# Performance work log

Hardware: AMD Instinct MI355X
Metric: run time of the kernel (lower is better)

The kernel has to match this reference:

```python
import jax, jax.numpy as jnp
import numpy as np
from jax import lax

B, FCH, H, W = 2, 48, 512, 512
WNUM, PATCH = 1, 8
DEG = 180.0 / np.pi
# well-conditioned, slightly asymmetric fallback Mueller matrix for masked (non-physical) pixels
_SAFE = np.array([[1.0, 0.02, 0.01, 0.005],
                  [0.0, 0.95, 0.05, 0.0],
                  [0.0, -0.05, 0.90, 0.04],
                  [0.0, 0.0, -0.04, 0.85]], dtype=np.float32)


def setup_inputs():
    key = jax.random.key(0)
    x = 0.5 * jax.random.normal(key, (B, FCH, H, W), dtype=jnp.float32)
    eye = jnp.eye(4, dtype=jnp.float32).reshape(16)
    # bias intensity frames and both calibration matrices toward 2*I so per-pixel
    # 4x4 systems are well conditioned and M is near-physical
    boost = jnp.concatenate([2.0 * eye, 2.0 * eye, 2.0 * eye])[None, :, None, None]
    return {"x": x + boost}


def _charpoly_mask(M):
    # Cloude realizability test: characteristic-polynomial coefficients of the
    # Hermitian coherency matrix must all be >= 0 (all eigenvalues >= 0).
    s = jnp.stack([jnp.eye(2, dtype=jnp.complex64),
                   jnp.array([[1, 0], [0, -1]], jnp.complex64),
                   jnp.array([[0, 1], [1, 0]], jnp.complex64),
                   jnp.array([[0, -1j], [1j, 0]], jnp.complex64)])
    Bk = jnp.einsum('iab,jcd->ijacbd', s, s).reshape(16, 4, 4)  # kron(sigma_i, sigma_j)
    Hc = 0.25 * jnp.einsum('...k,kab->...ab', M.reshape(M.shape[:-2] + (16,)).astype(jnp.complex64), Bk)
    tr1 = jnp.trace(Hc, axis1=-2, axis2=-1).real
    H2 = Hc @ Hc
    tr2 = jnp.trace(H2, axis1=-2, axis2=-1).real
    tr3 = jnp.trace(H2 @ Hc, axis1=-2, axis2=-1).real
    c2 = 0.5 * (tr1 ** 2 - tr2)
    c3 = (tr1 ** 3 - 3.0 * tr1 * tr2 + 2.0 * tr3) / 6.0
    c4 = jnp.linalg.det(Hc).real
    return (tr1 >= 0) & (c2 >= 0) & (c3 >= 0) & (c4 >= 0)


def _compute_mm(A, F, Wm, norm=True):
    M = jnp.linalg.solve(A, F)  # A^-1 F
    M = jnp.swapaxes(jnp.linalg.solve(jnp.swapaxes(Wm, -1, -2), jnp.swapaxes(M, -1, -2)), -1, -2)  # ... W^-1
    return M / M[..., 0:1, 0:1] if norm else M


def _lu_chipman(M, mask):
    # Lu-Chipman polar decomposition M = M_delta @ M_R @ M_D (per pixel)
    M = jnp.where(mask[..., None, None], M, jnp.asarray(_SAFE))
    I3 = jnp.eye(3, dtype=M.dtype)
    D = M[..., 0, 1:]  # diattenuation vector
    d2 = jnp.clip(jnp.sum(D * D, -1), 0.0, 1.0 - 1e-6)
    d = jnp.sqrt(d2 + 1e-12)
    sq = jnp.sqrt(1.0 - d2)
    Dh = D / jnp.maximum(d, 1e-6)[..., None]
    mD = sq[..., None, None] * I3 + (1.0 - sq)[..., None, None] * (Dh[..., :, None] * Dh[..., None, :])
    ones = jnp.ones(M.shape[:-2] + (1,), M.dtype)
    MD = jnp.concatenate([jnp.concatenate([ones, D], -1)[..., None, :],
                          jnp.concatenate([D[..., None], mD], -1)], -2)
    Mp = jnp.swapaxes(jnp.linalg.solve(MD, jnp.swapaxes(M, -1, -2)), -1, -2)  # M @ MD^-1 (MD symmetric)
    mp = Mp[..., 1:, 1:]
    mm = mp @ jnp.swapaxes(mp, -1, -2)
    lam = jnp.clip(jnp.linalg.eigvalsh(mm), 1e-12, None)  # ascending
    s1, s2, s3 = jnp.sqrt(lam[..., 2]), jnp.sqrt(lam[..., 1]), jnp.sqrt(lam[..., 0])
    sgn = jnp.where(jnp.linalg.det(mp) < 0, -1.0, 1.0).astype(M.dtype)
    A3 = mm + (s1 * s2 + s2 * s3 + s3 * s1)[..., None, None] * I3 + 1e-6 * I3
    B3 = (s1 + s2 + s3)[..., None, None] * mm + (s1 * s2 * s3)[..., None, None] * I3
    mdel = sgn[..., None, None] * jnp.linalg.solve(A3, B3)
    Pdel = (M[..., 1:, 0] - jnp.einsum('...ij,...j->...i', M[..., 1:, 1:], D)) / (1.0 - d2)[..., None]
    top = jnp.concatenate([ones, jnp.zeros(M.shape[:-2] + (3,), M.dtype)], -1)[..., None, :]
    Mdel = jnp.concatenate([top, jnp.concatenate([Pdel[..., None], mdel], -1)], -2)
    MR = jnp.linalg.solve(Mdel + 1e-6 * jnp.eye(4, dtype=M.dtype), Mp)
    return MD, MR, Mdel


def _polarimetry(MD, MR, Mdel):
    clipc = lambda t: jnp.clip(t, -1.0 + 1e-6, 1.0 - 1e-6)
    D = MD[..., 0, 1:]
    totD = jnp.sqrt(jnp.sum(D * D, -1) + 1e-12)
    linD = jnp.sqrt(D[..., 0] ** 2 + D[..., 1] ** 2 + 1e-12)
    cirD = jnp.abs(D[..., 2])
    totR = jnp.arccos(clipc(jnp.trace(MR, axis1=-2, axis2=-1) / 2.0 - 1.0)) * DEG
    mR = MR[..., 1:, 1:]
    linR = jnp.arccos(clipc(jnp.sqrt((mR[..., 0, 0] + mR[..., 1, 1]) ** 2
                                     + (mR[..., 1, 0] - mR[..., 0, 1]) ** 2 + 1e-12) - 1.0)) * DEG
    cirR = 0.5 * jnp.arctan2(mR[..., 1, 0] - mR[..., 0, 1], mR[..., 0, 0] + mR[..., 1, 1]) * DEG
    # azimuth of linear retardance from retardance-vector components (r1, r2)
    azi = jnp.mod(0.5 * jnp.arctan2(mR[..., 2, 0] - mR[..., 0, 2], mR[..., 1, 2] - mR[..., 2, 1]) * DEG, 180.0)
    dazi = jnp.mod(0.5 * jnp.arctan2(D[..., 1], D[..., 0]) * DEG, 180.0)
    totP = 1.0 - jnp.abs(jnp.trace(Mdel[..., 1:, 1:], axis1=-2, axis2=-1)) / 3.0
    # p[:,0]=diattenuation, p[:,6]=linear retardance, p[:,7]=azimuth, p[:,-1]=depolarization
    return jnp.stack([totD, linD, cirD, totR, cirR, dazi, linR, azi, totP], axis=1)


def _rolling_circstd(a_deg, patch):
    # circstd(a/180*pi, high=pi, low=0) over patch x patch sliding windows, back to degrees.
    # circstd reduces to window means of cos/sin of doubled angles -> avg pooling.
    th = a_deg * (2.0 * np.pi / 180.0)
    wsum = lambda t: lax.reduce_window(t, 0.0, lax.add, (1, 1, patch, patch), (1, 1, 1, 1), 'SAME')
    cnt = wsum(jnp.ones_like(a_deg))
    R = jnp.sqrt(wsum(jnp.cos(th)) ** 2 + wsum(jnp.sin(th)) ** 2 + 1e-12) / cnt
    R = jnp.clip(R, 1e-7, 1.0 - 1e-7)
    return 0.5 * jnp.sqrt(-2.0 * jnp.log(R)) * DEG


def _forward(x):
    b, f, h, w = x.shape
    xw = jnp.moveaxis(x.reshape(b, WNUM, f // WNUM, h, w), 2, -1)  # (b, wnum, h, w, 48)
    Fi = xw[..., :16].reshape(b, WNUM, h, w, 4, 4)
    Am = xw[..., 16:32].reshape(b, WNUM, h, w, 4, 4)
    Wm = xw[..., 32:48].reshape(b, WNUM, h, w, 4, 4)
    M = _compute_mm(Am, Fi, Wm, norm=True)
    inten = xw[..., 0]
    imin = inten.min(axis=(1, 2, 3), keepdims=True)
    imax = inten.max(axis=(1, 2, 3), keepdims=True)
    inorm = (inten - imin) / (imax - imin)
    mchan = jnp.moveaxis(M.reshape(b, WNUM, h, w, 16), -1, 2).reshape(b, WNUM * 16, h, w)
    v = lax.stop_gradient(_charpoly_mask(M))
    MD, MR, Mdel = _lu_chipman(M, v)
    p = _polarimetry(MD, MR, Mdel)  # (b, 9, wnum, h, w)
    std = _rolling_circstd(p[:, 7], PATCH)
    # concat order matches forward: intensity, mueller, linr, totp, datt, azimuth, std
    return jnp.concatenate([inorm, mchan, p[:, 6], p[:, 8], p[:, 0], p[:, 7], std], axis=1)


def reference(x):
    return _forward(x)
```

## Files before the change

kernel.cpp:

```cpp
#include <hip/hip_runtime.h>
#include <math.h>

#define B_ 2
#define H_ 512
#define W_ 512
#define HW_ (H_ * W_)
#define NCH_IN 48
#define NCH_OUT 22
#define DEG_ 57.29577951308232f

__device__ __forceinline__ float frcp(float x)  { return __builtin_amdgcn_rcpf(x); }
__device__ __forceinline__ float frcp_nr(float x) {
    float r = __builtin_amdgcn_rcpf(x);
    return r * __builtin_fmaf(-x, r, 2.0f);
}
__device__ __forceinline__ float fsqrtf_(float x){ return __builtin_amdgcn_sqrtf(x); }

__device__ __forceinline__ float fast_acos(float x) {
    float ax = fabsf(x);
    float t = fsqrtf_(fmaxf(1.0f - ax, 0.0f));
    float p = t * (1.5707288f + ax * (-0.2121144f + ax * (0.0742610f + ax * (-0.0187293f))));
    return (x >= 0.0f) ? p : (3.14159265358979f - p);
}

__device__ __forceinline__ float fast_atan2(float y, float x) {
    float ay = fabsf(y), ax = fabsf(x);
    float mx = fmaxf(ax, ay), mn = fminf(ax, ay);
    float a = mn * frcp(fmaxf(mx, 1e-37f));
    float s = a * a;
    float r = a * (0.99997726f + s * (-0.33262347f + s * (0.19354346f +
              s * (-0.11643287f + s * (0.05265332f + s * (-0.01172120f))))));
    if (ay > ax) r = 1.57079632679f - r;
    if (x < 0.0f) r = 3.14159265359f - r;
    return (y < 0.0f) ? -r : r;
}

__device__ __forceinline__ unsigned int fkey(float f) {
    unsigned int u = __float_as_uint(f);
    return (u & 0x80000000u) ? ~u : (u | 0x80000000u);
}
__device__ __forceinline__ float funkey(unsigned int k) {
    return (k & 0x80000000u) ? __uint_as_float(k ^ 0x80000000u) : __uint_as_float(~k);
}

__global__ __launch_bounds__(256) void minmax_kernel(const float* __restrict__ x,
                                                     unsigned int* __restrict__ mm) {
    int b = blockIdx.x >> 6;
    int blk = blockIdx.x & 63;
    const float* src = x + (size_t)b * NCH_IN * HW_;
    float lo = INFINITY, hi = -INFINITY;
    for (int i = blk * 256 + threadIdx.x; i < HW_; i += 64 * 256) {
        float v = src[i];
        lo = fminf(lo, v);
        hi = fmaxf(hi, v);
    }
    __shared__ float slo[256], shi[256];
    slo[threadIdx.x] = lo; shi[threadIdx.x] = hi;
    __syncthreads();
    for (int s = 128; s > 0; s >>= 1) {
        if (threadIdx.x < s) {
            slo[threadIdx.x] = fminf(slo[threadIdx.x], slo[threadIdx.x + s]);
            shi[threadIdx.x] = fmaxf(shi[threadIdx.x], shi[threadIdx.x + s]);
        }
        __syncthreads();
    }
    if (threadIdx.x == 0) {
        atomicMax(&mm[2 * b], ~fkey(slo[0]));
        atomicMax(&mm[2 * b + 1], fkey(shi[0]));
    }
}

__device__ __forceinline__ void solve4_dual(float m[2][4][8]) {
#pragma unroll
    for (int k = 0; k < 4; k++) {
#pragma unroll
        for (int r = k + 1; r < 4; r++) {
#pragma unroll
            for (int q = 0; q < 2; q++) {
                bool sw = fabsf(m[q][r][k]) > fabsf(m[q][k][k]);
#pragma unroll
                for (int c = k; c < 8; c++) {
                    float a = m[q][k][c], b = m[q][r][c];
                    m[q][k][c] = sw ? b : a;
                    m[q][r][c] = sw ? a : b;
                }
            }
        }
        float piv[2];
#pragma unroll
        for (int q = 0; q < 2; q++) piv[q] = frcp_nr(m[q][k][k]);
#pragma unroll
        for (int c = k + 1; c < 8; c++) {
#pragma unroll
            for (int q = 0; q < 2; q++) m[q][k][c] *= piv[q];
        }
#pragma unroll
        for (int r = 0; r < 4; r++) {
            if (r == k) continue;
#pragma unroll
            for (int q = 0; q < 2; q++) {
                float f = m[q][r][k];
#pragma unroll
                for (int c = k + 1; c < 8; c++)
                    m[q][r][c] = __builtin_fmaf(-f, m[q][k][c], m[q][r][c]);
            }
        }
    }
}

__device__ __forceinline__ void mul4(const float A[4][4], const float B[4][4], float C[4][4]) {
#pragma unroll
    for (int i = 0; i < 4; i++)
#pragma unroll
        for (int j = 0; j < 4; j++) {
            float s = 0.0f;
#pragma unroll
            for (int k = 0; k < 4; k++) s += A[i][k] * B[k][j];
            C[i][j] = s;
        }
}

__device__ __forceinline__ void inv3(const float A[3][3], float out[3][3]) {
    float c00 = A[1][1] * A[2][2] - A[1][2] * A[2][1];
    float c01 = A[1][2] * A[2][0] - A[1][0] * A[2][2];
    float c02 = A[1][0] * A[2][1] - A[1][1] * A[2][0];
    float det = A[0][0] * c00 + A[0][1] * c01 + A[0][2] * c02;
    float id = frcp_nr(det);
    out[0][0] = c00 * id;
    out[0][1] = (A[0][2] * A[2][1] - A[0][1] * A[2][2]) * id;
    out[0][2] = (A[0][1] * A[1][2] - A[0][2] * A[1][1]) * id;
    out[1][0] = c01 * id;
    out[1][1] = (A[0][0] * A[2][2] - A[0][2] * A[2][0]) * id;
    out[1][2] = (A[0][2] * A[1][0] - A[0][0] * A[1][2]) * id;
    out[2][0] = c02 * id;
    out[2][1] = (A[0][1] * A[2][0] - A[0][0] * A[2][1]) * id;
    out[2][2] = (A[0][0] * A[1][1] - A[0][1] * A[1][0]) * id;
}

__device__ __forceinline__ float det3(const float A[3][3]) {
    return A[0][0] * (A[1][1] * A[2][2] - A[1][2] * A[2][1])
         - A[0][1] * (A[1][0] * A[2][2] - A[1][2] * A[2][0])
         + A[0][2] * (A[1][0] * A[2][1] - A[1][1] * A[2][0]);
}

__device__ __forceinline__ void eig3_sym(const float A[3][3], float& l1, float& l2, float& l3) {
    float q = (A[0][0] + A[1][1] + A[2][2]) * (1.0f / 3.0f);
    float a00 = A[0][0] - q, a11 = A[1][1] - q, a22 = A[2][2] - q;
    float off = A[0][1] * A[0][1] + A[0][2] * A[0][2] + A[1][2] * A[1][2];
    float p2 = a00 * a00 + a11 * a11 + a22 * a22 + 2.0f * off;
    float p = fsqrtf_(p2 * (1.0f / 6.0f) + 1e-30f);
    float inv = frcp(p);
    float b00 = a00 * inv, b11 = a11 * inv, b22 = a22 * inv;
    float b01 = A[0][1] * inv, b02 = A[0][2] * inv, b12 = A[1][2] * inv;
    float detB = b00 * (b11 * b22 - b12 * b12)
               - b01 * (b01 * b22 - b12 * b02)
               + b02 * (b01 * b12 - b11 * b02);
    float r = 0.5f * detB;
    r = fminf(fmaxf(r, -1.0f), 1.0f);
    float phi = fast_acos(r) * (1.0f / 3.0f);
    l1 = q + 2.0f * p * __cosf(phi);
    l3 = q + 2.0f * p * __cosf(phi + 2.0943951023931953f);
    l2 = 3.0f * q - l1 - l3;
}

__device__ __forceinline__ void pixel_tail(float M[4][4], float inten,
                                           float imin, float imax, float* ob) {
    __builtin_nontemporal_store((inten - imin) * frcp(imax - imin), &ob[0]);
#pragma unroll
    for (int k = 0; k < 16; k++)
        __builtin_nontemporal_store(M[k >> 2][k & 3], &ob[(size_t)(1 + k) * HW_]);

    {
        float a0 = M[0][0], b0 = M[0][1], c0 = M[0][2], e0 = M[0][3];
        float a1 = M[1][0], b1 = M[1][1], c1 = M[1][2], e1 = M[1][3];
        float a2 = M[2][0], b2 = M[2][1], c2_ = M[2][2], e2 = M[2][3];
        float a3 = M[3][0], b3 = M[3][1], c3_ = M[3][2], e3 = M[3][3];
        float sa = a0 + a1, da = a0 - a1, sb = b0 + b1, db = b0 - b1;
        float d0 = sa + sb, d1 = sa - sb, d2 = da + db, d3 = da - db;
        float u01r = c0 + c1,  u01i = -(e0 + e1);
        float u23r = c0 - c1,  u23i = -(e0 - e1);
        float u02r = a2 + b2,  u02i = -(a3 + b3);
        float u13r = a2 - b2,  u13i = -(a3 - b3);
        float u03r = c2_ - e3, u03i = -(e2 + c3_);
        float u12r = c2_ + e3, u12i =  (e2 - c3_);

        float n01 = u01r * u01r + u01i * u01i;
        float n02 = u02r * u02r + u02i * u02i;
        float n03 = u03r * u03r + u03i * u03i;
        float n12 = u12r * u12r + u12i * u12i;
        float n13 = u13r * u13r + u13i * u13i;
        float n23 = u23r * u23r + u23i * u23i;

        float q0 = d0 * d0 + n01 + n02 + n03;
        float q1 = d1 * d1 + n01 + n12 + n13;
        float q2 = d2 * d2 + n02 + n12 + n23;
        float q3 = d3 * d3 + n03 + n13 + n23;
        float p2 = q0 + q1 + q2 + q3;

        float w01r = (d0 + d1) * u01r + (u02r * u12r + u02i * u12i) + (u03r * u13r + u03i * u13i);
        float w01i = (d0 + d1) * u01i + (u02i * u12r - u02r * u12i) + (u03i * u13r - u03r * u13i);
        float w02r = (d0 + d2) * u02r + (u01r * u12r - u01i * u12i) + (u03r * u23r + u03i * u23i);
        float w02i = (d0 + d2) * u02i + (u01r * u12i + u01i * u12r) + (u03i * u23r - u03r * u23i);
        float w03r = (d0 + d3) * u03r + (u01r * u13r - u01i * u13i) + (u02r * u23r - u02i * u23i);
        float w03i = (d0 + d3) * u03i + (u01r * u13i + u01i * u13r) + (u02r * u23i + u02i * u23r);
        float w12r = (d1 + d2) * u12r + (u01r * u02r + u01i * u02i) + (u13r * u23r + u13i * u23i);
        float w12i = (d1 + d2) * u12i + (u01r * u02i - u01i * u02r) + (u13i * u23r - u13r * u23i);
        float w13r = (d1 + d3) * u13r + (u01r * u03r + u01i * u03i) + (u12r * u23r - u12i * u23i);
        float w13i = (d1 + d3) * u13i + (u01r * u03i - u01i * u03r) + (u12r * u23i + u12i * u23r);
        float w23r = (d2 + d3) * u23r + (u02r * u03r + u02i * u03i) + (u12r * u13r + u12i * u13i);
        float w23i = (d2 + d3) * u23i + (u02r * u03i - u02i * u03r) + (u12i * u13r - u12r * u13i);

        float p3 = q0 * d0 + q1 * d1 + q2 * d2 + q3 * d3
                 + 2.0f * (w01r * u01r + w01i * u01i + w02r * u02r + w02i * u02i
                         + w03r * u03r + w03i * u03i + w12r * u12r + w12i * u12i
                         + w13r * u13r + w13i * u13i + w23r * u23r + w23i * u23i);
        float p4 = q0 * q0 + q1 * q1 + q2 * q2 + q3 * q3
                 + 2.0f * (w01r * w01r + w01i * w01i + w02r * w02r + w02i * w02i
                         + w03r * w03r + w03i * w03i + w12r * w12r + w12i * w12i
                         + w13r * w13r + w13i * w13i + w23r * w23r + w23i * w23i);

        float tr1 = 4.0f * a0;
        float t2 = tr1 * tr1;
        float c2v = t2 - p2;
        float c3v = tr1 * t2 - 3.0f * tr1 * p2 + 2.0f * p3;
        float c4v = t2 * t2 - 6.0f * t2 * p2 + 3.0f * p2 * p2 + 8.0f * tr1 * p3 - 6.0f * p4;
        bool mask = (tr1 >= 0.0f) && (c2v >= 0.0f) && (c3v >= 0.0f) && (c4v >= 0.0f);

        const float SAFE[4][4] = {{1.0f, 0.02f, 0.01f, 0.005f},
                                  {0.0f, 0.95f, 0.05f, 0.0f},
                                  {0.0f, -0.05f, 0.9f, 0.04f},
                                  {0.0f, 0.0f, -0.04f, 0.85f}};
#pragma unroll
        for (int i = 0; i < 4; i++)
#pragma unroll
            for (int j = 0; j < 4; j++) M[i][j] = mask ? M[i][j] : SAFE[i][j];
    }

    float D0 = M[0][1], D1 = M[0][2], D2v = M[0][3];
    float d2r = D0 * D0 + D1 * D1 + D2v * D2v;
    float totD = fsqrtf_(d2r + 1e-12f);
    float d2 = fminf(fmaxf(d2r, 0.0f), 1.0f - 1e-6f);
    float d = fsqrtf_(d2 + 1e-12f);
    float sq2 = 1.0f - d2;
    float sq = fsqrtf_(sq2);
    float dinv = frcp(fmaxf(d, 1e-6f));
    float h0 = D0 * dinv, h1 = D1 * dinv, h2 = D2v * dinv;

    float isq2 = frcp_nr(sq2);
    float isq = frcp(sq);
    float cdh = (1.0f - sq) * isq2;
    float MDi[4][4];
    MDi[0][0] = isq2;
    MDi[0][1] = -isq2 * D0; MDi[0][2] = -isq2 * D1; MDi[0][3] = -isq2 * D2v;
    MDi[1][0] = MDi[0][1];  MDi[2][0] = MDi[0][2];  MDi[3][0] = MDi[0][3];
    float Dh[3] = {h0, h1, h2};
#pragma unroll
    for (int i = 0; i < 3; i++)
#pragma unroll
        for (int j = 0; j < 3; j++)
            MDi[1 + i][1 + j] = ((i == j) ? isq : 0.0f) + cdh * Dh[i] * Dh[j];

    float Mp[4][4];
    mul4(M, MDi, Mp);

    float mp3[3][3];
#pragma unroll
    for (int i = 0; i < 3; i++)
#pragma unroll
        for (int j = 0; j < 3; j++) mp3[i][j] = Mp[1 + i][1 + j];
    float mmS[3][3];
#pragma unroll
    for (int i = 0; i < 3; i++)
#pragma unroll
        for (int j = 0; j < 3; j++) {
            float s = 0.0f;
#pragma unroll
            for (int k = 0; k < 3; k++) s += mp3[i][k] * mp3[j][k];
            mmS[i][j] = s;
        }
    float l1, l2, l3;
    eig3_sym(mmS, l1, l2, l3);
    l1 = fmaxf(l1, 1e-12f); l2 = fmaxf(l2, 1e-12f); l3 = fmaxf(l3, 1e-12f);
    float s1 = fsqrtf_(l1), s2 = fsqrtf_(l2), s3 = fsqrtf_(l3);
    float sgn = (det3(mp3) < 0.0f) ? -1.0f : 1.0f;

    float e2s = s1 * s2 + s2 * s3 + s3 * s1 + 1e-6f;
    float e1s = s1 + s2 + s3;
    float e3s = s1 * s2 * s3;
    float A3[3][3], B3[3][3];
#pragma unroll
    for (int i = 0; i < 3; i++)
#pragma unroll
        for (int j = 0; j < 3; j++) {
            A3[i][j] = mmS[i][j] + ((i == j) ? e2s : 0.0f);
            B3[i][j] = e1s * mmS[i][j] + ((i == j) ? e3s : 0.0f);
        }
    float A3i[3][3];
    inv3(A3, A3i);
    float mdel[3][3];
#pragma unroll
    for (int i = 0; i < 3; i++)
#pragma unroll
        for (int j = 0; j < 3; j++) {
            float s = 0.0f;
#pragma unroll
            for (int k = 0; k < 3; k++) s += A3i[i][k] * B3[k][j];
            mdel[i][j] = sgn * s;
        }

    float Pd[3];
#pragma unroll
    for (int i = 0; i < 3; i++)
        Pd[i] = (M[1 + i][0] - (M[1 + i][1] * D0 + M[1 + i][2] * D1 + M[1 + i][3] * D2v)) * isq2;

    float MR0[4];
    const float inv_aeps = 1.0f / (1.0f + 1e-6f);
#pragma unroll
    for (int j = 0; j < 4; j++) MR0[j] = Mp[0][j] * inv_aeps;
    float m3[3][3];
#pragma unroll
    for (int i = 0; i < 3; i++)
#pragma unroll
        for (int j = 0; j < 3; j++) m3[i][j] = mdel[i][j] + ((i == j) ? 1e-6f : 0.0f);
    float m3i[3][3];
    inv3(m3, m3i);
    float MRr[3][4];
#pragma unroll
    for (int i = 0; i < 3; i++)
#pragma unroll
        for (int j = 0; j < 4; j++) {
            float s = 0.0f;
#pragma unroll
            for (int k = 0; k < 3; k++) s += m3i[i][k] * (Mp[1 + k][j] - Pd[k] * MR0[j]);
            MRr[i][j] = s;
        }

    float mR00 = MRr[0][1], mR01 = MRr[0][2], mR02 = MRr[0][3];
    float mR10 = MRr[1][1], mR11 = MRr[1][2], mR12 = MRr[1][3];
    float mR20 = MRr[2][1], mR21 = MRr[2][2];

    float t_lin = fsqrtf_((mR00 + mR11) * (mR00 + mR11) + (mR10 - mR01) * (mR10 - mR01) + 1e-12f) - 1.0f;
    t_lin = fminf(fmaxf(t_lin, -1.0f + 1e-6f), 1.0f - 1e-6f);
    float linR = fast_acos(t_lin) * DEG_;

    float azi = 0.5f * fast_atan2(mR20 - mR02, mR12 - mR21) * DEG_;
    if (azi < 0.0f) azi += 180.0f;

    float totP = 1.0f - fabsf(mdel[0][0] + mdel[1][1] + mdel[2][2]) * (1.0f / 3.0f);

    __builtin_nontemporal_store(linR, &ob[(size_t)17 * HW_]);
    __builtin_nontemporal_store(totP, &ob[(size_t)18 * HW_]);
    __builtin_nontemporal_store(totD, &ob[(size_t)19 * HW_]);
    ob[(size_t)20 * HW_] = azi;
}

__global__ __launch_bounds__(256) void main_kernel(const float* __restrict__ x,
                                                   const unsigned int* __restrict__ mmk,
                                                   float* __restrict__ out) {
    int idx = blockIdx.x * 256 + threadIdx.x;

    float m[2][4][8];
    float WT[2][4][4];
    float inten[2];
#pragma unroll
    for (int q = 0; q < 2; q++) {
        const float* src = x + (size_t)q * NCH_IN * HW_ + idx;
#pragma unroll
        for (int i = 0; i < 4; i++)
#pragma unroll
            for (int j = 0; j < 4; j++) {
                m[q][i][4 + j] = __builtin_nontemporal_load(&src[(4 * i + j) * HW_]);
                m[q][i][j]     = __builtin_nontemporal_load(&src[(16 + 4 * i + j) * HW_]);
                WT[q][j][i]    = __builtin_nontemporal_load(&src[(32 + 4 * i + j) * HW_]);
            }
        inten[q] = m[q][0][4];
    }

    solve4_dual(m);

    float m2[2][4][8];
#pragma unroll
    for (int q = 0; q < 2; q++)
#pragma unroll
        for (int i = 0; i < 4; i++)
#pragma unroll
            for (int j = 0; j < 4; j++) {
                m2[q][i][j]     = WT[q][i][j];
                m2[q][i][4 + j] = m[q][j][4 + i];
            }
    solve4_dual(m2);

    float M[2][4][4];
#pragma unroll
    for (int q = 0; q < 2; q++) {
        float nrm = frcp_nr(m2[q][0][4]);
#pragma unroll
        for (int i = 0; i < 4; i++)
#pragma unroll
            for (int j = 0; j < 4; j++) M[q][i][j] = m2[q][j][4 + i] * nrm;
    }

#pragma unroll
    for (int q = 0; q < 2; q++) {
        float* ob = out + (size_t)q * NCH_OUT * HW_ + idx;
        float imin = funkey(~mmk[2 * q]), imax = funkey(mmk[2 * q + 1]);
        pixel_tail(M[q], inten[q], imin, imax, ob);
    }
}

#define TX_ 32
#define TY_ 8
__global__ __launch_bounds__(256) void circstd_kernel(float* __restrict__ out) {
    int tx0 = blockIdx.x * TX_;
    int ty0 = blockIdx.y * TY_;
    int b = blockIdx.z;
    const float* azi = out + (size_t)b * NCH_OUT * HW_ + (size_t)20 * HW_;

    __shared__ float lc[TY_ + 7][TX_ + 8];
    __shared__ float ls[TY_ + 7][TX_ + 8];
    __shared__ float hc[TY_ + 7][TX_];
    __shared__ float hs[TY_ + 7][TX_];

    for (int i = threadIdx.x; i < (TY_ + 7) * (TX_ + 7); i += 256) {
        int row = i / (TX_ + 7);
        int col = i - row * (TX_ + 7);
        int gy = ty0 - 3 + row;
        int gx = tx0 - 3 + col;
        float c = 0.0f, s = 0.0f;
        if (gy >= 0 && gy < H_ && gx >= 0 && gx < W_) {
            float th = azi[(size_t)gy * W_ + gx] * 0.03490658503988659f;
            __sincosf(th, &s, &c);
        }
        lc[row][col] = c; ls[row][col] = s;
    }
    __syncthreads();

    for (int i = threadIdx.x; i < (TY_ + 7) * TX_; i += 256) {
        int row = i / TX_;
        int col = i - row * TX_;
        float sc = 0.0f, ss = 0.0f;
#pragma unroll
        for (int d = 0; d < 8; d++) { sc += lc[row][col + d]; ss += ls[row][col + d]; }
        hc[row][col] = sc; hs[row][col] = ss;
    }
    __syncthreads();

    int col = threadIdx.x & (TX_ - 1);
    int row = threadIdx.x >> 5;
    float sc = 0.0f, ss = 0.0f;
#pragma unroll
    for (int k = 0; k < 8; k++) { sc += hc[row + k][col]; ss += hs[row + k][col]; }
    int y = ty0 + row, xc = tx0 + col;
    float rows = (float)(min(y + 5, H_) - max(y - 3, 0));
    float cols = (float)(min(xc + 5, W_) - max(xc - 3, 0));
    float R = fsqrtf_(sc * sc + ss * ss + 1e-12f) * frcp(rows * cols);
    R = fminf(fmaxf(R, 1e-7f), 1.0f - 1e-7f);
    float stdv = 0.5f * fsqrtf_(-2.0f * __logf(R)) * DEG_;
    __builtin_nontemporal_store(stdv,
        &out[(size_t)b * NCH_OUT * HW_ + (size_t)21 * HW_ + (size_t)y * W_ + xc]);
}

extern "C" void kernel_launch(void* const* d_in, const int* in_sizes, int n_in,
                              void* d_out, int out_size, void* d_ws, size_t ws_size,
                              hipStream_t stream) {
    const float* x = (const float*)d_in[0];
    float* out = (float*)d_out;
    unsigned int* mmk = (unsigned int*)d_ws;

    hipMemsetAsync(mmk, 0, 4 * sizeof(unsigned int), stream);
    hipLaunchKernelGGL(minmax_kernel, dim3(128), dim3(256), 0, stream, x, mmk);
    hipLaunchKernelGGL(main_kernel, dim3(HW_ / 256), dim3(256), 0, stream, x, mmk, out);
    hipLaunchKernelGGL(circstd_kernel, dim3(W_ / TX_, H_ / TY_, B_), dim3(256), 0, stream, out);
}
```

Measured before the change: 171.6 us.

## Remap main kernel to two adjacent pixels per thread with vector loads/stores

Before, each thread took one pixel index and handled that pixel for both batches. Now each thread takes two horizontally adjacent pixels of the same batch, so every channel load and store becomes a 2-wide vector access. The min/max reduction is also changed to read float4 with half as many blocks. The aim is fewer memory instructions and wider transactions. The cost is that pixel_tail now runs its heavy code for two pixels at once, which raises register pressure, and the grid size stays the same.

```diff
diff --git a/kernel.cpp b/kernel.cpp
--- a/kernel.cpp
+++ b/kernel.cpp
@@ -8,6 +8,8 @@
 #define NCH_IN 48
 #define NCH_OUT 22
 #define DEG_ 57.29577951308232f
+
+typedef float f2 __attribute__((ext_vector_type(2)));
 
 __device__ __forceinline__ float frcp(float x)  { return __builtin_amdgcn_rcpf(x); }
 __device__ __forceinline__ float frcp_nr(float x) {
@@ -45,14 +47,14 @@
 
 __global__ __launch_bounds__(256) void minmax_kernel(const float* __restrict__ x,
                                                      unsigned int* __restrict__ mm) {
-    int b = blockIdx.x >> 6;
-    int blk = blockIdx.x & 63;
-    const float* src = x + (size_t)b * NCH_IN * HW_;
+    int b = blockIdx.x >> 5;
+    int blk = blockIdx.x & 31;
+    const float4* src = (const float4*)(x + (size_t)b * NCH_IN * HW_);
     float lo = INFINITY, hi = -INFINITY;
-    for (int i = blk * 256 + threadIdx.x; i < HW_; i += 64 * 256) {
-        float v = src[i];
-        lo = fminf(lo, v);
-        hi = fmaxf(hi, v);
+    for (int i = blk * 256 + threadIdx.x; i < HW_ / 4; i += 32 * 256) {
+        float4 v = src[i];
+        lo = fminf(lo, fminf(fminf(v.x, v.y), fminf(v.z, v.w)));
+        hi = fmaxf(hi, fmaxf(fmaxf(v.x, v.y), fmaxf(v.z, v.w)));
     }
     __shared__ float slo[256], shi[256];
     slo[threadIdx.x] = lo; shi[threadIdx.x] = hi;
@@ -163,13 +165,8 @@
     l2 = 3.0f * q - l1 - l3;
 }
 
-__device__ __forceinline__ void pixel_tail(float M[4][4], float inten,
-                                           float imin, float imax, float* ob) {
-    __builtin_nontemporal_store((inten - imin) * frcp(imax - imin), &ob[0]);
-#pragma unroll
-    for (int k = 0; k < 16; k++)
-        __builtin_nontemporal_store(M[k >> 2][k & 3], &ob[(size_t)(1 + k) * HW_]);
-
+__device__ __forceinline__ void pixel_tail(float M[4][4], float& linR_o, float& totP_o,
+                                           float& totD_o, float& azi_o) {
     {
         float a0 = M[0][0], b0 = M[0][1], c0 = M[0][2], e0 = M[0][3];
         float a1 = M[1][0], b1 = M[1][1], c1 = M[1][2], e1 = M[1][3];
@@ -348,44 +345,43 @@
 
     float totP = 1.0f - fabsf(mdel[0][0] + mdel[1][1] + mdel[2][2]) * (1.0f / 3.0f);
 
-    __builtin_nontemporal_store(linR, &ob[(size_t)17 * HW_]);
-    __builtin_nontemporal_store(totP, &ob[(size_t)18 * HW_]);
-    __builtin_nontemporal_store(totD, &ob[(size_t)19 * HW_]);
-    ob[(size_t)20 * HW_] = azi;
+    linR_o = linR; totP_o = totP; totD_o = totD; azi_o = azi;
 }
 
 __global__ __launch_bounds__(256) void main_kernel(const float* __restrict__ x,
                                                    const unsigned int* __restrict__ mmk,
                                                    float* __restrict__ out) {
-    int idx = blockIdx.x * 256 + threadIdx.x;
+    int tid = blockIdx.x * 256 + threadIdx.x;
+    int b = tid / (HW_ / 2);
+    int pp = tid - b * (HW_ / 2);
+    int p = pp * 2;
+    const float* src = x + (size_t)b * NCH_IN * HW_ + p;
 
     float m[2][4][8];
-    float WT[2][4][4];
-    float inten[2];
-#pragma unroll
-    for (int q = 0; q < 2; q++) {
-        const float* src = x + (size_t)q * NCH_IN * HW_ + idx;
+    float Wv[2][4][4];
+#pragma unroll
+    for (int i = 0; i < 4; i++)
+#pragma unroll
+        for (int j = 0; j < 4; j++) {
+            f2 f = __builtin_nontemporal_load((const f2*)&src[(size_t)(4 * i + j) * HW_]);
+            f2 a = __builtin_nontemporal_load((const f2*)&src[(size_t)(16 + 4 * i + j) * HW_]);
+            f2 w = __builtin_nontemporal_load((const f2*)&src[(size_t)(32 + 4 * i + j) * HW_]);
+            m[0][i][4 + j] = f.x; m[1][i][4 + j] = f.y;
+            m[0][i][j]     = a.x; m[1][i][j]     = a.y;
+            Wv[0][j][i]    = w.x; Wv[1][j][i]    = w.y;
+        }
+    float inten0 = m[0][0][4], inten1 = m[1][0][4];
+
+    solve4_dual(m);
+
+    float m2[2][4][8];
+#pragma unroll
+    for (int q = 0; q < 2; q++)
 #pragma unroll
         for (int i = 0; i < 4; i++)
 #pragma unroll
             for (int j = 0; j < 4; j++) {
-                m[q][i][4 + j] = __builtin_nontemporal_load(&src[(4 * i + j) * HW_]);
-                m[q][i][j]     = __builtin_nontemporal_load(&src[(16 + 4 * i + j) * HW_]);
-                WT[q][j][i]    = __builtin_nontemporal_load(&src[(32 + 4 * i + j) * HW_]);
-            }
-        inten[q] = m[q][0][4];
-    }
-
-    solve4_dual(m);
-
-    float m2[2][4][8];
-#pragma unroll
-    for (int q = 0; q < 2; q++)
-#pragma unroll
-        for (int i = 0; i < 4; i++)
-#pragma unroll
-            for (int j = 0; j < 4; j++) {
-                m2[q][i][j]     = WT[q][i][j];
+                m2[q][i][j]     = Wv[q][i][j];
                 m2[q][i][4 + j] = m[q][j][4 + i];
             }
     solve4_dual(m2);
@@ -400,12 +396,29 @@
             for (int j = 0; j < 4; j++) M[q][i][j] = m2[q][j][4 + i] * nrm;
     }
 
-#pragma unroll
-    for (int q = 0; q < 2; q++) {
-        float* ob = out + (size_t)q * NCH_OUT * HW_ + idx;
-        float imin = funkey(~mmk[2 * q]), imax = funkey(mmk[2 * q + 1]);
-        pixel_tail(M[q], inten[q], imin, imax, ob);
-    }
+    float* ob = out + (size_t)b * NCH_OUT * HW_ + p;
+    float imin = funkey(~mmk[2 * b]), imax = funkey(mmk[2 * b + 1]);
+    float iscale = frcp(imax - imin);
+    {
+        f2 v; v.x = (inten0 - imin) * iscale; v.y = (inten1 - imin) * iscale;
+        __builtin_nontemporal_store(v, (f2*)&ob[0]);
+    }
+#pragma unroll
+    for (int k = 0; k < 16; k++) {
+        f2 v; v.x = M[0][k >> 2][k & 3]; v.y = M[1][k >> 2][k & 3];
+        __builtin_nontemporal_store(v, (f2*)&ob[(size_t)(1 + k) * HW_]);
+    }
+
+    float linR[2], totP[2], totD[2], azi[2];
+#pragma unroll
+    for (int q = 0; q < 2; q++)
+        pixel_tail(M[q], linR[q], totP[q], totD[q], azi[q]);
+
+    f2 v;
+    v.x = linR[0]; v.y = linR[1]; __builtin_nontemporal_store(v, (f2*)&ob[(size_t)17 * HW_]);
+    v.x = totP[0]; v.y = totP[1]; __builtin_nontemporal_store(v, (f2*)&ob[(size_t)18 * HW_]);
+    v.x = totD[0]; v.y = totD[1]; __builtin_nontemporal_store(v, (f2*)&ob[(size_t)19 * HW_]);
+    v.x = azi[0];  v.y = azi[1];  *(f2*)&ob[(size_t)20 * HW_] = v;
 }
 
 #define TX_ 32
@@ -468,7 +481,7 @@
     unsigned int* mmk = (unsigned int*)d_ws;
 
     hipMemsetAsync(mmk, 0, 4 * sizeof(unsigned int), stream);
-    hipLaunchKernelGGL(minmax_kernel, dim3(128), dim3(256), 0, stream, x, mmk);
-    hipLaunchKernelGGL(main_kernel, dim3(HW_ / 256), dim3(256), 0, stream, x, mmk, out);
+    hipLaunchKernelGGL(minmax_kernel, dim3(64), dim3(256), 0, stream, x, mmk);
+    hipLaunchKernelGGL(main_kernel, dim3(B_ * HW_ / 2 / 256), dim3(256), 0, stream, x, mmk, out);
     hipLaunchKernelGGL(circstd_kernel, dim3(W_ / TX_, H_ / TY_, B_), dim3(256), 0, stream, out);
 }
```

Result: faster. 166.2 us (-3.1%).
